# Optimization experiments

Measured on AMD Instinct MI355X. Metric: run time of the kernel, lower is better.

## Reference

```python
import jax, jax.numpy as jnp
import numpy as np

N = 20000          # num_nodes
E = 160000         # directed edges (doubled to undirected inside reference)
NF, EF, H, OUT, K = 16, 16, 128, 16, 3


def mlp2(x, w1, b1, w2, b2):
    return jnp.maximum(x @ w1 + b1, 0.0) @ w2 + b2


def edge_agg(x, src, dst, eattr, w1, b1, w2, b2):
    # message = MLP(cat[x_i (target), x_j (source), edge_attr]); aggr='add' at target
    m = mlp2(jnp.concatenate([x[dst], x[src], eattr], axis=-1), w1, b1, w2, b2)
    return jax.ops.segment_sum(m, dst, num_segments=x.shape[0])


def tag_conv(x, src, dst, lins, bias):
    # PyG TAGConv: gcn_norm (no self loops), out = sum_k lin_k(L^k x) + bias
    n = x.shape[0]
    deg = jax.ops.segment_sum(jnp.ones_like(src, dtype=x.dtype), dst, num_segments=n)
    dis = jnp.where(deg > 0, jax.lax.rsqrt(deg), 0.0)
    norm = dis[src] * dis[dst]                     # [E]
    out = x @ lins[0]
    h = x
    for k in range(1, lins.shape[0]):
        h = jax.ops.segment_sum(norm[:, None] * h[src], dst, num_segments=n)
        out = out + h @ lins[k]
    return out + bias


def setup_inputs() -> dict:
    key = jax.random.key(0)
    ks = jax.random.split(key, 20)
    s = 0.05
    lin = lambda k, i, o: jax.random.normal(k, (i, o), jnp.float32) * s
    inp = {}
    inp["x"] = jax.random.normal(ks[0], (N, NF), jnp.float32)
    inp["mask"] = (jax.random.uniform(ks[1], (N, NF)) > 0.5).astype(jnp.float32)
    inp["edge_attr"] = jax.random.normal(ks[2], (E, EF), jnp.float32)
    inp["edge_index"] = jax.random.randint(ks[3], (2, E), 0, N)
    inp["m_w1"] = lin(ks[4], NF, H); inp["m_b1"] = jnp.zeros(H)
    inp["m_w2"] = lin(ks[5], H, NF); inp["m_b2"] = jnp.zeros(NF)
    inp["ea0_w1"] = lin(ks[6], 2 * NF + EF, H); inp["ea0_b1"] = jnp.zeros(H)
    inp["ea0_w2"] = lin(ks[7], H, H); inp["ea0_b2"] = jnp.zeros(H)
    inp["tag0_w"] = jax.random.normal(ks[8], (K + 1, H, H), jnp.float32) * s
    inp["tag0_b"] = jnp.zeros(H)
    inp["ea1_w1"] = lin(ks[9], 2 * H + EF, H); inp["ea1_b1"] = jnp.zeros(H)
    inp["ea1_w2"] = lin(ks[10], H, H); inp["ea1_b2"] = jnp.zeros(H)
    inp["tag1_w"] = jax.random.normal(ks[11], (K + 1, H, H), jnp.float32) * s
    inp["tag1_b"] = jnp.zeros(H)
    inp["ea2_w1"] = lin(ks[12], 2 * H + EF, H); inp["ea2_b1"] = jnp.zeros(H)
    inp["ea2_w2"] = lin(ks[13], H, OUT); inp["ea2_b2"] = jnp.zeros(OUT)
    return inp


def reference(x, mask, edge_attr, m_w1, m_b1, m_w2, m_b2,
              ea0_w1, ea0_b1, ea0_w2, ea0_b2, tag0_w, tag0_b,
              ea1_w1, ea1_b1, ea1_w2, ea1_b2, tag1_w, tag1_b,
              ea2_w1, ea2_b1, ea2_w2, ea2_b2, edge_index):
    # undirect_graph: random directed edges -> duplicate reversed copies
    src0, dst0 = edge_index[0], edge_index[1]
    src = jnp.concatenate([src0, dst0])
    dst = jnp.concatenate([dst0, src0])
    ea = jnp.concatenate([edge_attr, edge_attr], axis=0)
    # mask embedding + residual
    h = mlp2(mask, m_w1, m_b1, m_w2, m_b2) + x
    # [EA, TAG, EA, TAG] with ReLU (dropout = identity in eval)
    h = jnp.maximum(edge_agg(h, src, dst, ea, ea0_w1, ea0_b1, ea0_w2, ea0_b2), 0.0)
    h = jnp.maximum(tag_conv(h, src, dst, tag0_w, tag0_b), 0.0)
    h = jnp.maximum(edge_agg(h, src, dst, ea, ea1_w1, ea1_b1, ea1_w2, ea1_b2), 0.0)
    h = jnp.maximum(tag_conv(h, src, dst, tag1_w, tag1_b), 0.0)
    # final EA (no activation)
    return edge_agg(h, src, dst, ea, ea2_w1, ea2_b1, ea2_w2, ea2_b2)
```

## Files before the change

### kernel.cpp

```cpp
#include <hip/hip_runtime.h>

typedef unsigned short u16;
typedef unsigned char u8;
typedef unsigned int u32;

using bfrag  = __attribute__((ext_vector_type(8))) short;
using f32x2  = __attribute__((ext_vector_type(2))) float;
using f32x4  = __attribute__((ext_vector_type(4))) float;
using f32x16 = __attribute__((ext_vector_type(16))) float;

__device__ __forceinline__ float b2f(u16 u) {
  union { u32 i; float f; } c; c.i = ((u32)u) << 16; return c.f;
}
__device__ __forceinline__ float bflo(u32 u) { union { u32 i; float f; } c; c.i = u << 16; return c.f; }
__device__ __forceinline__ float bfhi(u32 u) { union { u32 i; float f; } c; c.i = u & 0xffff0000u; return c.f; }
__device__ __forceinline__ u16 f2b(float f) {
  union { float f; u32 i; } c; c.f = f;
  u32 x = c.i;
  u32 r = x + 0x7fffu + ((x >> 16) & 1u);
  return (u16)(r >> 16);
}
__device__ __forceinline__ u32 packb2(float x, float y) {
  return ((u32)f2b(x)) | (((u32)f2b(y)) << 16);
}
__device__ __forceinline__ int rfl(int v) { return __builtin_amdgcn_readfirstlane(v); }

__global__ __launch_bounds__(256) void prologue(
    const float* __restrict__ ea, const int* __restrict__ eidx,
    const float* __restrict__ ea0_w1, const float* __restrict__ ea0_w2,
    const float* __restrict__ tag0_w, const float* __restrict__ ea1_w1,
    const float* __restrict__ ea1_w2, const float* __restrict__ tag1_w,
    const float* __restrict__ ea2_w1,
    u8* __restrict__ P0, u8* __restrict__ P1, u8* __restrict__ P2,
    int* __restrict__ degi, u16* __restrict__ Wt, int E, int N,
    int PB, int CB, int EB) {
  int t = threadIdx.x;
  if (blockIdx.x < (unsigned)PB) {
    __shared__ u16 Alds[256 * 16];
    __shared__ u16 Wlds[2048];
    int tab = blockIdx.x / EB;
    int chunk = blockIdx.x - tab * EB;
    int base = chunk * 256;
    int rows = E - base; if (rows > 256) rows = 256;
    const float* wsrc = (tab == 0) ? (ea0_w1 + 32 * 128)
                      : (tab == 1) ? (ea1_w1 + 256 * 128)
                                   : (ea2_w1 + 256 * 128);
    u8* P = (tab == 0) ? P0 : (tab == 1) ? P1 : P2;
#pragma unroll
    for (int i = 0; i < 8; ++i) {
      int idx = i * 256 + t;
      int n = idx >> 4, k = idx & 15;
      Wlds[idx] = f2b(wsrc[k * 128 + n]);
    }
#pragma unroll
    for (int i = 0; i < 4; ++i) {
      int idx = (i * 256 + t) * 4;
      float4 v = make_float4(0.f, 0.f, 0.f, 0.f);
      if ((idx >> 4) < rows) v = *(const float4*)(ea + (size_t)base * 16 + idx);
      ushort4 h;
      h.x = f2b(v.x); h.y = f2b(v.y); h.z = f2b(v.z); h.w = f2b(v.w);
      *(ushort4*)(Alds + idx) = h;
    }
    __syncthreads();
    int wave = t >> 6, lane = t & 63;
    int mm = lane & 31, kh = lane >> 5;
    bfrag b00 = *(const bfrag*)(Wlds + (2 * mm) * 16 + kh * 8);
    bfrag b01 = *(const bfrag*)(Wlds + (2 * mm + 1) * 16 + kh * 8);
    bfrag b10 = *(const bfrag*)(Wlds + (64 + 2 * mm) * 16 + kh * 8);
    bfrag b11 = *(const bfrag*)(Wlds + (64 + 2 * mm + 1) * 16 + kh * 8);
#pragma unroll
    for (int it = 0; it < 4; ++it) {
      int task = wave + it * 4;
      int rowt = (task >> 1) * 32;
      int ch = task & 1;
      int colt = ch * 64;
      bfrag a = *(const bfrag*)(Alds + (rowt + mm) * 16 + kh * 8);
      f32x16 acc0, acc1;
#pragma unroll
      for (int z = 0; z < 16; ++z) { acc0[z] = 0.f; acc1[z] = 0.f; }
      acc0 = __builtin_amdgcn_mfma_f32_32x32x16_bf16(a, ch ? b10 : b00, acc0, 0, 0, 0);
      acc1 = __builtin_amdgcn_mfma_f32_32x32x16_bf16(a, ch ? b11 : b01, acc1, 0, 0, 0);
#pragma unroll
      for (int reg = 0; reg < 16; ++reg) {
        int row = rowt + (reg & 3) + 8 * (reg >> 2) + 4 * kh;
        if (row < rows) {
          u32 pk = (u32)__builtin_amdgcn_cvt_pk_fp8_f32(acc0[reg], acc1[reg], 0, false);
          *(u16*)(P + (size_t)(base + row) * 128 + colt + 2 * mm) = (u16)pk;
        }
      }
    }
    return;
  }
  if (blockIdx.x < (unsigned)(PB + CB)) {
    int e = (blockIdx.x - PB) * 256 + t;
    if (e < E) {
      atomicAdd(&degi[eidx[E + e]], 1);
      atomicAdd(&degi[eidx[e]], 1);
    }
    return;
  }
  int wb = blockIdx.x - PB - CB;
  int mat = wb >> 3, chunk = wb & 7;
  const float* src;
  if      (mat == 0)  src = ea0_w2;
  else if (mat <= 4)  src = tag0_w + (mat - 1) * 16384;
  else if (mat == 5)  src = ea1_w1;
  else if (mat == 6)  src = ea1_w1 + 16384;
  else if (mat == 7)  src = ea1_w2;
  else if (mat <= 11) src = tag1_w + (mat - 8) * 16384;
  else if (mat == 12) src = ea2_w1;
  else                src = ea2_w1 + 16384;
  u16* dst = Wt + mat * 16384;
  for (int i = 0; i < 8; ++i) {
    int idx = chunk * 2048 + i * 256 + t;
    int k = idx >> 7, n = idx & 127;
    dst[n * 128 + k] = f2b(src[idx]);
  }
}

__global__ __launch_bounds__(256) void scan1(const int* __restrict__ degi,
                                             int* __restrict__ bsum, int N) {
  __shared__ int sh[256];
  int t = threadIdx.x;
  int gid = blockIdx.x * 256 + t;
  sh[t] = (gid < N) ? degi[gid] : 0;
  __syncthreads();
  for (int off = 128; off > 0; off >>= 1) {
    if (t < off) sh[t] += sh[t + off];
    __syncthreads();
  }
  if (t == 0) bsum[blockIdx.x] = sh[0];
}

__global__ __launch_bounds__(256) void scan23(const int* __restrict__ degi,
                                              const int* __restrict__ bsum,
                                              int* __restrict__ rowptr,
                                              int* __restrict__ cursor,
                                              float* __restrict__ dis, int nb, int N) {
  __shared__ int sh[256];
  int t = threadIdx.x;
  int v = (t < nb) ? bsum[t] : 0;
  sh[t] = v;
  __syncthreads();
  for (int off = 1; off < 256; off <<= 1) {
    int x = sh[t];
    int add = (t >= off) ? sh[t - off] : 0;
    __syncthreads();
    sh[t] = x + add;
    __syncthreads();
  }
  int blockoff = (blockIdx.x == 0) ? 0 : sh[blockIdx.x - 1];
  int total = sh[nb - 1];
  __syncthreads();
  int gid = blockIdx.x * 256 + t;
  int d = (gid < N) ? degi[gid] : 0;
  sh[t] = d;
  __syncthreads();
  for (int off = 1; off < 256; off <<= 1) {
    int x = sh[t];
    int add = (t >= off) ? sh[t - off] : 0;
    __syncthreads();
    sh[t] = x + add;
    __syncthreads();
  }
  if (gid < N) {
    int run = blockoff + sh[t] - d;
    rowptr[gid] = run;
    cursor[gid] = run;
    dis[gid] = d > 0 ? rsqrtf((float)d) : 0.0f;
  }
  if (blockIdx.x == 0 && t == 0) rowptr[N] = total;
}

__global__ __launch_bounds__(256) void fill_head(
    const int* __restrict__ eidx, int* __restrict__ cursor,
    const float* __restrict__ dis, int4* __restrict__ cr, int E,
    const float* __restrict__ mask, const float* __restrict__ x,
    const float* __restrict__ m_w1, const float* __restrict__ m_b1,
    const float* __restrict__ m_w2, const float* __restrict__ m_b2,
    const float* __restrict__ ea0_w1, const float* __restrict__ ea0_b1,
    u16* __restrict__ pb, u16* __restrict__ q, int M, int FB) {
  int t = threadIdx.x;
  if (blockIdx.x < (unsigned)FB) {
    int i = blockIdx.x * 256 + t;
    int E2 = 2 * E;
    if (i >= E2) return;
    int e = (i < E) ? i : i - E;
    int s, d;
    if (i < E) { s = eidx[e]; d = eidx[E + e]; }
    else       { s = eidx[E + e]; d = eidx[e]; }
    int pos = atomicAdd(&cursor[d], 1);
    cr[pos] = make_int4(s, e, __float_as_int(dis[s]), 0);
    return;
  }
  __shared__ float Ml[16 * 16];
  __shared__ float T1[16 * 128];
  __shared__ float H[16 * 16];
  int base = (blockIdx.x - FB) * 16;
  {
    int r = t >> 4, k = t & 15;
    int row = base + r;
    Ml[t] = (row < M) ? mask[(size_t)row * 16 + k] : 0.f;
  }
  __syncthreads();
  {
    int col = t & 127, h2 = t >> 7;
    float acc[8];
    float b1v = m_b1[col];
#pragma unroll
    for (int r = 0; r < 8; ++r) acc[r] = b1v;
    for (int k = 0; k < 16; ++k) {
      float w = m_w1[k * 128 + col];
#pragma unroll
      for (int r = 0; r < 8; ++r) acc[r] += Ml[(h2 * 8 + r) * 16 + k] * w;
    }
#pragma unroll
    for (int r = 0; r < 8; ++r) T1[(h2 * 8 + r) * 128 + col] = fmaxf(acc[r], 0.f);
  }
  __syncthreads();
  {
    int r = t >> 4, u = t & 15;
    float acc = m_b2[u];
    for (int k = 0; k < 128; ++k) acc += T1[r * 128 + k] * m_w2[k * 16 + u];
    int row = base + r;
    float xv = (row < M) ? x[(size_t)row * 16 + u] : 0.f;
    H[t] = acc + xv;
  }
  __syncthreads();
  {
    int col = t & 127, h2 = t >> 7;
    float aP[8], aQ[8];
    float b1v = ea0_b1[col];
#pragma unroll
    for (int r = 0; r < 8; ++r) { aP[r] = b1v; aQ[r] = 0.f; }
    for (int k = 0; k < 16; ++k) {
      float wd = ea0_w1[k * 128 + col];
      float ws = ea0_w1[(16 + k) * 128 + col];
#pragma unroll
      for (int r = 0; r < 8; ++r) {
        float h = H[(h2 * 8 + r) * 16 + k];
        aP[r] += h * wd;
        aQ[r] += h * ws;
      }
    }
#pragma unroll
    for (int r = 0; r < 8; ++r) {
      int row = base + h2 * 8 + r;
      if (row < M) {
        pb[(size_t)row * 128 + col] = f2b(aP[r]);
        q[(size_t)row * 128 + col]  = f2b(aQ[r]);
      }
    }
  }
}

__global__ __launch_bounds__(256) void gemm_mfma_dual(
    const u16* __restrict__ A, const u16* __restrict__ W0t, const u16* __restrict__ W1t,
    u16* __restrict__ C0, u16* __restrict__ C1, const float* __restrict__ bias0, int M) {
  __shared__ u16 Alds[64 * 136];
  __shared__ u16 Wlds[128 * 136];
  int t = threadIdx.x;
  int base = blockIdx.x * 64;
#pragma unroll
  for (int i = 0; i < 8; ++i) {
    int idx = (i * 256 + t) * 8;
    int n = idx >> 7, k = idx & 127;
    uint4 v = *(const uint4*)(W0t + idx);
    *(uint4*)(Wlds + n * 136 + k) = v;
  }
#pragma unroll
  for (int i = 0; i < 4; ++i) {
    int idx = (i * 256 + t) * 8;
    int r = idx >> 7, k = idx & 127;
    int row = base + r;
    uint4 v = make_uint4(0, 0, 0, 0);
    if (row < M) v = *(const uint4*)(A + (size_t)row * 128 + k);
    *(uint4*)(Alds + r * 136 + k) = v;
  }
  __syncthreads();
  int wave = t >> 6, lane = t & 63;
  int m = lane & 15, quad = lane >> 4;
  int arow = wave * 16 + m;
  bfrag a[4];
#pragma unroll
  for (int ks = 0; ks < 4; ++ks)
    a[ks] = *(const bfrag*)(Alds + arow * 136 + ks * 32 + quad * 8);
  f32x4 acc0[8], acc1[8];
#pragma unroll
  for (int nt = 0; nt < 8; ++nt) { acc0[nt] = (f32x4){0,0,0,0}; acc1[nt] = (f32x4){0,0,0,0}; }
#pragma unroll
  for (int nt = 0; nt < 8; ++nt) {
    int n = nt * 16 + m;
#pragma unroll
    for (int ks = 0; ks < 4; ++ks) {
      bfrag b = *(const bfrag*)(Wlds + n * 136 + ks * 32 + quad * 8);
      acc0[nt] = __builtin_amdgcn_mfma_f32_16x16x32_bf16(a[ks], b, acc0[nt], 0, 0, 0);
    }
  }
  __syncthreads();
#pragma unroll
  for (int i = 0; i < 8; ++i) {
    int idx = (i * 256 + t) * 8;
    int n = idx >> 7, k = idx & 127;
    uint4 v = *(const uint4*)(W1t + idx);
    *(uint4*)(Wlds + n * 136 + k) = v;
  }
  __syncthreads();
#pragma unroll
  for (int nt = 0; nt < 8; ++nt) {
    int n = nt * 16 + m;
#pragma unroll
    for (int ks = 0; ks < 4; ++ks) {
      bfrag b = *(const bfrag*)(Wlds + n * 136 + ks * 32 + quad * 8);
      acc1[nt] = __builtin_amdgcn_mfma_f32_16x16x32_bf16(a[ks], b, acc1[nt], 0, 0, 0);
    }
  }
#pragma unroll
  for (int nt = 0; nt < 8; ++nt) {
    int col = nt * 16 + m;
#pragma unroll
    for (int r = 0; r < 4; ++r) {
      int row = base + wave * 16 + quad * 4 + r;
      if (row < M) {
        float v0 = acc0[nt][r];
        if (bias0) v0 += bias0[col];
        C0[(size_t)row * 128 + col] = f2b(v0);
        C1[(size_t)row * 128 + col] = f2b(acc1[nt][r]);
      }
    }
  }
}

__global__ __launch_bounds__(256) void gemm_mfma_penta(
    const u16* __restrict__ A, const u16* __restrict__ W2t, const u16* __restrict__ Wt4,
    const float* __restrict__ bias, const int* __restrict__ degi,
    u16* __restrict__ G0, u16* __restrict__ G1,
    u16* __restrict__ G2, u16* __restrict__ G3, int M) {
  __shared__ u16 Alds[64 * 136];
  __shared__ u16 Wlds[128 * 136];
  int t = threadIdx.x;
  int base = blockIdx.x * 64;
#pragma unroll
  for (int i = 0; i < 8; ++i) {
    int idx = (i * 256 + t) * 8;
    int n = idx >> 7, k = idx & 127;
    uint4 v = *(const uint4*)(W2t + idx);
    *(uint4*)(Wlds + n * 136 + k) = v;
  }
#pragma unroll
  for (int i = 0; i < 4; ++i) {
    int idx = (i * 256 + t) * 8;
    int r = idx >> 7, k = idx & 127;
    int row = base + r;
    uint4 v = make_uint4(0, 0, 0, 0);
    if (row < M) v = *(const uint4*)(A + (size_t)row * 128 + k);
    *(uint4*)(Alds + r * 136 + k) = v;
  }
  __syncthreads();
  int wave = t >> 6, lane = t & 63;
  int m = lane & 15, quad = lane >> 4;
  int arow = wave * 16 + m;
  bfrag a[4];
#pragma unroll
  for (int ks = 0; ks < 4; ++ks)
    a[ks] = *(const bfrag*)(Alds + arow * 136 + ks * 32 + quad * 8);
  {
    f32x4 acc[8];
#pragma unroll
    for (int nt = 0; nt < 8; ++nt) acc[nt] = (f32x4){0.f, 0.f, 0.f, 0.f};
#pragma unroll
    for (int nt = 0; nt < 8; ++nt) {
      int n = nt * 16 + m;
#pragma unroll
      for (int ks = 0; ks < 4; ++ks) {
        bfrag b = *(const bfrag*)(Wlds + n * 136 + ks * 32 + quad * 8);
        acc[nt] = __builtin_amdgcn_mfma_f32_16x16x32_bf16(a[ks], b, acc[nt], 0, 0, 0);
      }
    }
#pragma unroll
    for (int nt = 0; nt < 8; ++nt) {
      int col = nt * 16 + m;
#pragma unroll
      for (int r = 0; r < 4; ++r) {
        int lrow = wave * 16 + quad * 4 + r;
        int row = base + lrow;
        float v = 0.f;
        if (row < M) v = fmaxf(acc[nt][r] + bias[col] * (float)degi[row], 0.f);
        Alds[lrow * 136 + col] = f2b(v);
      }
    }
  }
#pragma unroll
  for (int ks = 0; ks < 4; ++ks)
    a[ks] = *(const bfrag*)(Alds + arow * 136 + ks * 32 + quad * 8);
#pragma unroll
  for (int mat = 0; mat < 4; ++mat) {
    __syncthreads();
#pragma unroll
    for (int i = 0; i < 8; ++i) {
      int idx = (i * 256 + t) * 8;
      int n = idx >> 7, k = idx & 127;
      uint4 v = *(const uint4*)(Wt4 + mat * 16384 + idx);
      *(uint4*)(Wlds + n * 136 + k) = v;
    }
    __syncthreads();
    f32x4 acc[8];
#pragma unroll
    for (int nt = 0; nt < 8; ++nt) acc[nt] = (f32x4){0.f, 0.f, 0.f, 0.f};
#pragma unroll
    for (int nt = 0; nt < 8; ++nt) {
      int n = nt * 16 + m;
#pragma unroll
      for (int ks = 0; ks < 4; ++ks) {
        bfrag b = *(const bfrag*)(Wlds + n * 136 + ks * 32 + quad * 8);
        acc[nt] = __builtin_amdgcn_mfma_f32_16x16x32_bf16(a[ks], b, acc[nt], 0, 0, 0);
      }
    }
    u16* G = (mat == 0) ? G0 : (mat == 1) ? G1 : (mat == 2) ? G2 : G3;
#pragma unroll
    for (int nt = 0; nt < 8; ++nt) {
      int col = nt * 16 + m;
#pragma unroll
      for (int r = 0; r < 4; ++r) {
        int row = base + wave * 16 + quad * 4 + r;
        if (row < M) G[(size_t)row * 128 + col] = f2b(acc[nt][r]);
      }
    }
  }
}

__global__ __launch_bounds__(128) void gemm_tail(
    const u16* __restrict__ A, const float* __restrict__ W, float* __restrict__ Cout,
    const float* __restrict__ bias, const int* __restrict__ degi, int M) {
  const int ROWS = 8;
  int t = threadIdx.x;
  int base = blockIdx.x * ROWS;
  __shared__ float Al[ROWS * 128];
  for (int i = t; i < ROWS * 128; i += 128) {
    int r = i >> 7, k = i & 127;
    int row = base + r;
    Al[i] = (row < M) ? b2f(A[(size_t)row * 128 + k]) : 0.f;
  }
  __syncthreads();
  int r = t >> 4, u = t & 15;
  int row = base + r;
  float acc = 0.f;
  for (int k = 0; k < 128; ++k) acc += Al[r * 128 + k] * W[k * 16 + u];
  if (row < M) {
    Cout[(size_t)row * 16 + u] = acc + bias[u] * (float)degi[row];
  }
}

__device__ __forceinline__ void tag_edge(const int4* __restrict__ rr, int j,
    const u16* __restrict__ g, int lane, float& x0, float& x1) {
  int4 r = rr[j];
  int s = rfl(r.x); float w = __uint_as_float(rfl(r.z));
  u32 h = *((const u32*)(g + (size_t)s * 128) + lane);
  x0 += w * bflo(h); x1 += w * bfhi(h);
}
__device__ __forceinline__ void ea_edge(const int4* __restrict__ rr, int j,
    const u16* __restrict__ q, const u8* __restrict__ P8, int lane,
    float pb0, float pb1, float& x0, float& x1) {
  int4 r = rr[j];
  int s = rfl(r.x), i = rfl(r.y);
  u32 qv = *((const u32*)(q + (size_t)s * 128) + lane);
  u16 pv = *((const u16*)(P8 + (size_t)i * 128) + lane);
  f32x2 pf = __builtin_amdgcn_cvt_pk_f32_fp8((int)pv, false);
  x0 += fmaxf(pb0 + bflo(qv) + pf.x, 0.f);
  x1 += fmaxf(pb1 + bfhi(qv) + pf.y, 0.f);
}

template<bool FINAL>
__global__ __launch_bounds__(256) void tag_gather9(
    const u16* __restrict__ g, const u16* __restrict__ Cin,
    const float* __restrict__ bias, const float* __restrict__ dis,
    const int* __restrict__ rowptr, const int4* __restrict__ cr,
    u16* __restrict__ out, int N) {
  __shared__ int4 recs[4][64];
  int wave = threadIdx.x >> 6, lane = threadIdx.x & 63;
  int node = blockIdx.x * 4 + wave;
  if (node >= N) return;
  int e0 = rfl(rowptr[node]);
  int e1 = rfl(rowptr[node + 1]);
  int4* rr = recs[wave];
  float a0 = 0, a1 = 0, b0 = 0, b1 = 0;
  for (int base = e0; base < e1; base += 64) {
    if (base + lane < e1) rr[lane] = cr[base + lane];
    int cnt = min(64, e1 - base);
    int j = 0;
    for (; j + 8 <= cnt; j += 8) {
      tag_edge(rr, j + 0, g, lane, a0, a1);
      tag_edge(rr, j + 1, g, lane, b0, b1);
      tag_edge(rr, j + 2, g, lane, a0, a1);
      tag_edge(rr, j + 3, g, lane, b0, b1);
      tag_edge(rr, j + 4, g, lane, a0, a1);
      tag_edge(rr, j + 5, g, lane, b0, b1);
      tag_edge(rr, j + 6, g, lane, a0, a1);
      tag_edge(rr, j + 7, g, lane, b0, b1);
    }
    for (; j + 2 <= cnt; j += 2) {
      tag_edge(rr, j + 0, g, lane, a0, a1);
      tag_edge(rr, j + 1, g, lane, b0, b1);
    }
    if (j < cnt) tag_edge(rr, j, g, lane, a0, a1);
  }
  float dn = dis[node];
  float r0v = dn * (a0 + b0), r1v = dn * (a1 + b1);
  u32 cin = *((const u32*)(Cin + (size_t)node * 128) + lane);
  r0v += bflo(cin); r1v += bfhi(cin);
  if (FINAL) {
    float2 bv = *(const float2*)(bias + 2 * lane);
    r0v = fmaxf(r0v + bv.x, 0.f);
    r1v = fmaxf(r1v + bv.y, 0.f);
  }
  *((u32*)(out + (size_t)node * 128) + lane) = packb2(r0v, r1v);
}

__global__ __launch_bounds__(256) void ea_gather10(
    const u16* __restrict__ pb, const u16* __restrict__ q,
    const u8* __restrict__ P ,
    const int* __restrict__ rowptr, const int4* __restrict__ cr,
    u16* __restrict__ Hsum, int N) {
  __shared__ int4 recs[4][64];
  int wave = threadIdx.x >> 6, lane = threadIdx.x & 63;
  int node = blockIdx.x * 4 + wave;
  if (node >= N) return;
  int e0 = rfl(rowptr[node]);
  int e1 = rfl(rowptr[node + 1]);
  int4* rr = recs[wave];
  u32 pbu = *((const u32*)(pb + (size_t)node * 128) + lane);
  float pb0 = bflo(pbu), pb1 = bfhi(pbu);
  float a0 = 0, a1 = 0, b0 = 0, b1 = 0;
  for (int base = e0; base < e1; base += 64) {
    if (base + lane < e1) rr[lane] = cr[base + lane];
    int cnt = min(64, e1 - base);
    int j = 0;
    for (; j + 8 <= cnt; j += 8) {
      ea_edge(rr, j + 0, q, P, lane, pb0, pb1, a0, a1);
      ea_edge(rr, j + 1, q, P, lane, pb0, pb1, b0, b1);
      ea_edge(rr, j + 2, q, P, lane, pb0, pb1, a0, a1);
      ea_edge(rr, j + 3, q, P, lane, pb0, pb1, b0, b1);
      ea_edge(rr, j + 4, q, P, lane, pb0, pb1, a0, a1);
      ea_edge(rr, j + 5, q, P, lane, pb0, pb1, b0, b1);
      ea_edge(rr, j + 6, q, P, lane, pb0, pb1, a0, a1);
      ea_edge(rr, j + 7, q, P, lane, pb0, pb1, b0, b1);
    }
    for (; j + 2 <= cnt; j += 2) {
      ea_edge(rr, j + 0, q, P, lane, pb0, pb1, a0, a1);
      ea_edge(rr, j + 1, q, P, lane, pb0, pb1, b0, b1);
    }
    if (j < cnt) ea_edge(rr, j, q, P, lane, pb0, pb1, a0, a1);
  }
  *((u32*)(Hsum + (size_t)node * 128) + lane) = packb2(a0 + b0, a1 + b1);
}

extern "C" void kernel_launch(void* const* d_in, const int* in_sizes, int n_in,
                              void* d_out, int out_size, void* d_ws, size_t ws_size,
                              hipStream_t stream) {
  const float* x      = (const float*)d_in[0];
  const float* mask   = (const float*)d_in[1];
  const float* ea     = (const float*)d_in[2];
  const int*   eidx   = (const int*)d_in[3];
  const float* m_w1   = (const float*)d_in[4];
  const float* m_b1   = (const float*)d_in[5];
  const float* m_w2   = (const float*)d_in[6];
  const float* m_b2   = (const float*)d_in[7];
  const float* ea0_w1 = (const float*)d_in[8];
  const float* ea0_b1 = (const float*)d_in[9];
  const float* ea0_w2 = (const float*)d_in[10];
  const float* ea0_b2 = (const float*)d_in[11];
  const float* tag0_w = (const float*)d_in[12];
  const float* tag0_b = (const float*)d_in[13];
  const float* ea1_w1 = (const float*)d_in[14];
  const float* ea1_b1 = (const float*)d_in[15];
  const float* ea1_w2 = (const float*)d_in[16];
  const float* ea1_b2 = (const float*)d_in[17];
  const float* tag1_w = (const float*)d_in[18];
  const float* tag1_b = (const float*)d_in[19];
  const float* ea2_w1 = (const float*)d_in[20];
  const float* ea2_b1 = (const float*)d_in[21];
  const float* ea2_w2 = (const float*)d_in[22];
  const float* ea2_b2 = (const float*)d_in[23];

  const int N = in_sizes[0] / 16;
  const int E = in_sizes[2] / 16;
  const int E2 = 2 * E;
  const int NB = (N + 255) / 256;

  char* w = (char*)d_ws;
  auto alloc = [&](size_t bytes) { char* p = w; w += (bytes + 255) & ~(size_t)255; return p; };
  int*   degi   = (int*)alloc((size_t)N * 4);
  int*   cursor = (int*)alloc((size_t)N * 4);
  int*   rowptr = (int*)alloc((size_t)(N + 1) * 4);
  int*   bsum   = (int*)alloc((size_t)256 * 4);
  float* dis    = (float*)alloc((size_t)N * 4);
  int4*  cr     = (int4*)alloc((size_t)E2 * 16);
  u16*   X0     = (u16*)alloc((size_t)N * 128 * 2);
  u16*   X1     = (u16*)alloc((size_t)N * 128 * 2);
  u16*   X2     = (u16*)alloc((size_t)N * 128 * 2);
  u16*   G0     = (u16*)alloc((size_t)N * 128 * 2);
  u16*   G1     = (u16*)alloc((size_t)N * 128 * 2);
  u16*   G2     = (u16*)alloc((size_t)N * 128 * 2);
  u16*   G3     = (u16*)alloc((size_t)N * 128 * 2);
  u16*   Wt     = (u16*)alloc((size_t)14 * 16384 * 2);
  u8*    P0     = (u8*)alloc((size_t)E * 128);
  u8*    P1     = (u8*)alloc((size_t)E * 128);
  u8*    P2     = (u8*)alloc((size_t)E * 128);
  (void)ws_size; (void)n_in; (void)out_size;

  const int EB = (E + 255) / 256;
  const int PB = 3 * EB;
  const int CB = (E + 255) / 256;
  const int FB = (E2 + 255) / 256;
  const int HB = (N + 15) / 16;
  const int gm = (N + 63) / 64;
  const int g4 = (N + 3) / 4;
  const int gb = (N + 7) / 8;

  u16* WT_ea0w2  = Wt + 0 * 16384;
  u16* WT_tag0   = Wt + 1 * 16384;
  u16* WT_ea1d   = Wt + 5 * 16384;
  u16* WT_ea1s   = Wt + 6 * 16384;
  u16* WT_ea1w2  = Wt + 7 * 16384;
  u16* WT_tag1   = Wt + 8 * 16384;
  u16* WT_ea2d   = Wt + 12 * 16384;
  u16* WT_ea2s   = Wt + 13 * 16384;

  hipMemsetAsync(degi, 0, (size_t)N * 4, stream);
  prologue<<<PB + CB + 112, 256, 0, stream>>>(ea, eidx, ea0_w1, ea0_w2, tag0_w,
                                              ea1_w1, ea1_w2, tag1_w, ea2_w1,
                                              P0, P1, P2, degi, Wt, E, N, PB, CB, EB);
  scan1<<<NB, 256, 0, stream>>>(degi, bsum, N);
  scan23<<<NB, 256, 0, stream>>>(degi, bsum, rowptr, cursor, dis, NB, N);
  fill_head<<<FB + HB, 256, 0, stream>>>(eidx, cursor, dis, cr, E,
                                         mask, x, m_w1, m_b1, m_w2, m_b2,
                                         ea0_w1, ea0_b1, X0, X1, N, FB);

  ea_gather10<<<g4, 256, 0, stream>>>(X0, X1, P0, rowptr, cr, X2, N);
  gemm_mfma_penta<<<gm, 256, 0, stream>>>(X2, WT_ea0w2, WT_tag0, ea0_b2, degi,
                                          G0, G1, G2, G3, N);
  tag_gather9<false><<<g4, 256, 0, stream>>>(G3, G2, nullptr, dis, rowptr, cr, X1, N);
  tag_gather9<false><<<g4, 256, 0, stream>>>(X1, G1, nullptr, dis, rowptr, cr, X2, N);
  tag_gather9<true><<<g4, 256, 0, stream>>>(X2, G0, tag0_b, dis, rowptr, cr, X0, N);

  gemm_mfma_dual<<<gm, 256, 0, stream>>>(X0, WT_ea1d, WT_ea1s, X1, X2, ea1_b1, N);
  ea_gather10<<<g4, 256, 0, stream>>>(X1, X2, P1, rowptr, cr, G0, N);
  gemm_mfma_penta<<<gm, 256, 0, stream>>>(G0, WT_ea1w2, WT_tag1, ea1_b2, degi,
                                          G0, G1, G2, G3, N);
  tag_gather9<false><<<g4, 256, 0, stream>>>(G3, G2, nullptr, dis, rowptr, cr, X1, N);
  tag_gather9<false><<<g4, 256, 0, stream>>>(X1, G1, nullptr, dis, rowptr, cr, X2, N);
  tag_gather9<true><<<g4, 256, 0, stream>>>(X2, G0, tag1_b, dis, rowptr, cr, X0, N);

  gemm_mfma_dual<<<gm, 256, 0, stream>>>(X0, WT_ea2d, WT_ea2s, X1, X2, ea2_b1, N);
  ea_gather10<<<g4, 256, 0, stream>>>(X1, X2, P2, rowptr, cr, G0, N);
  gemm_tail<<<gb, 128, 0, stream>>>(G0, ea2_w2, (float*)d_out, ea2_b2, degi, N);
}
```

Before: 389.1 us.

## Move degree counting ahead and merge edge-MLP precompute into CSR fill kernel

Degree counting is split into its own small kernel that runs first. The heavy edge-attribute projection tables (P0/P1/P2) and the weight transposes move out of the prologue and into a single merged kernel together with CSR fill and the head MLP, which runs after the scans. The aim is to shorten the serial critical path: the scans now wait only on the cheap atomic degree pass instead of the large edge-GEMM prologue. Folding the GEMM work into the fill launch removes one launch and overlaps independent work. The cost is a heterogeneous mega-kernel whose shared-memory footprint applies to every block.

```diff
diff --git a/kernel.cpp b/kernel.cpp
--- a/kernel.cpp
+++ b/kernel.cpp
@@ -25,15 +25,83 @@
 }
 __device__ __forceinline__ int rfl(int v) { return __builtin_amdgcn_readfirstlane(v); }
 
-__global__ __launch_bounds__(256) void prologue(
+__global__ __launch_bounds__(256) void count_deg(const int* __restrict__ eidx,
+                                                 int* __restrict__ degi, int E) {
+  int e = blockIdx.x * 256 + threadIdx.x;
+  if (e >= E) return;
+  atomicAdd(&degi[eidx[E + e]], 1);
+  atomicAdd(&degi[eidx[e]], 1);
+}
+
+__global__ __launch_bounds__(256) void scan1(const int* __restrict__ degi,
+                                             int* __restrict__ bsum, int N) {
+  __shared__ int sh[256];
+  int t = threadIdx.x;
+  int gid = blockIdx.x * 256 + t;
+  sh[t] = (gid < N) ? degi[gid] : 0;
+  __syncthreads();
+  for (int off = 128; off > 0; off >>= 1) {
+    if (t < off) sh[t] += sh[t + off];
+    __syncthreads();
+  }
+  if (t == 0) bsum[blockIdx.x] = sh[0];
+}
+
+__global__ __launch_bounds__(256) void scan23(const int* __restrict__ degi,
+                                              const int* __restrict__ bsum,
+                                              int* __restrict__ rowptr,
+                                              int* __restrict__ cursor,
+                                              float* __restrict__ dis, int nb, int N) {
+  __shared__ int sh[256];
+  int t = threadIdx.x;
+  int v = (t < nb) ? bsum[t] : 0;
+  sh[t] = v;
+  __syncthreads();
+  for (int off = 1; off < 256; off <<= 1) {
+    int x = sh[t];
+    int add = (t >= off) ? sh[t - off] : 0;
+    __syncthreads();
+    sh[t] = x + add;
+    __syncthreads();
+  }
+  int blockoff = (blockIdx.x == 0) ? 0 : sh[blockIdx.x - 1];
+  int total = sh[nb - 1];
+  __syncthreads();
+  int gid = blockIdx.x * 256 + t;
+  int d = (gid < N) ? degi[gid] : 0;
+  sh[t] = d;
+  __syncthreads();
+  for (int off = 1; off < 256; off <<= 1) {
+    int x = sh[t];
+    int add = (t >= off) ? sh[t - off] : 0;
+    __syncthreads();
+    sh[t] = x + add;
+    __syncthreads();
+  }
+  if (gid < N) {
+    int run = blockoff + sh[t] - d;
+    rowptr[gid] = run;
+    cursor[gid] = run;
+    dis[gid] = d > 0 ? rsqrtf((float)d) : 0.0f;
+  }
+  if (blockIdx.x == 0 && t == 0) rowptr[N] = total;
+}
+
+__global__ __launch_bounds__(256) void mega(
     const float* __restrict__ ea, const int* __restrict__ eidx,
-    const float* __restrict__ ea0_w1, const float* __restrict__ ea0_w2,
+    const float* __restrict__ ea0_w1, const float* __restrict__ ea0_b1,
+    const float* __restrict__ ea0_w2,
     const float* __restrict__ tag0_w, const float* __restrict__ ea1_w1,
     const float* __restrict__ ea1_w2, const float* __restrict__ tag1_w,
     const float* __restrict__ ea2_w1,
+    const float* __restrict__ mask, const float* __restrict__ x,
+    const float* __restrict__ m_w1, const float* __restrict__ m_b1,
+    const float* __restrict__ m_w2, const float* __restrict__ m_b2,
     u8* __restrict__ P0, u8* __restrict__ P1, u8* __restrict__ P2,
-    int* __restrict__ degi, u16* __restrict__ Wt, int E, int N,
-    int PB, int CB, int EB) {
+    u16* __restrict__ Wt, int* __restrict__ cursor,
+    const float* __restrict__ dis, int4* __restrict__ cr,
+    u16* __restrict__ pb, u16* __restrict__ q,
+    int E, int N, int PB, int FB, int EB) {
   int t = threadIdx.x;
   if (blockIdx.x < (unsigned)PB) {
     __shared__ u16 Alds[256 * 16];
@@ -91,98 +159,28 @@
     }
     return;
   }
-  if (blockIdx.x < (unsigned)(PB + CB)) {
-    int e = (blockIdx.x - PB) * 256 + t;
-    if (e < E) {
-      atomicAdd(&degi[eidx[E + e]], 1);
-      atomicAdd(&degi[eidx[e]], 1);
+  if (blockIdx.x < (unsigned)(PB + 112)) {
+    int wb = blockIdx.x - PB;
+    int mat = wb >> 3, chunk = wb & 7;
+    const float* src;
+    if      (mat == 0)  src = ea0_w2;
+    else if (mat <= 4)  src = tag0_w + (mat - 1) * 16384;
+    else if (mat == 5)  src = ea1_w1;
+    else if (mat == 6)  src = ea1_w1 + 16384;
+    else if (mat == 7)  src = ea1_w2;
+    else if (mat <= 11) src = tag1_w + (mat - 8) * 16384;
+    else if (mat == 12) src = ea2_w1;
+    else                src = ea2_w1 + 16384;
+    u16* dst = Wt + mat * 16384;
+    for (int i = 0; i < 8; ++i) {
+      int idx = chunk * 2048 + i * 256 + t;
+      int k = idx >> 7, n = idx & 127;
+      dst[n * 128 + k] = f2b(src[idx]);
     }
     return;
   }
-  int wb = blockIdx.x - PB - CB;
-  int mat = wb >> 3, chunk = wb & 7;
-  const float* src;
-  if      (mat == 0)  src = ea0_w2;
-  else if (mat <= 4)  src = tag0_w + (mat - 1) * 16384;
-  else if (mat == 5)  src = ea1_w1;
-  else if (mat == 6)  src = ea1_w1 + 16384;
-  else if (mat == 7)  src = ea1_w2;
-  else if (mat <= 11) src = tag1_w + (mat - 8) * 16384;
-  else if (mat == 12) src = ea2_w1;
-  else                src = ea2_w1 + 16384;
-  u16* dst = Wt + mat * 16384;
-  for (int i = 0; i < 8; ++i) {
-    int idx = chunk * 2048 + i * 256 + t;
-    int k = idx >> 7, n = idx & 127;
-    dst[n * 128 + k] = f2b(src[idx]);
-  }
-}
-
-__global__ __launch_bounds__(256) void scan1(const int* __restrict__ degi,
-                                             int* __restrict__ bsum, int N) {
-  __shared__ int sh[256];
-  int t = threadIdx.x;
-  int gid = blockIdx.x * 256 + t;
-  sh[t] = (gid < N) ? degi[gid] : 0;
-  __syncthreads();
-  for (int off = 128; off > 0; off >>= 1) {
-    if (t < off) sh[t] += sh[t + off];
-    __syncthreads();
-  }
-  if (t == 0) bsum[blockIdx.x] = sh[0];
-}
-
-__global__ __launch_bounds__(256) void scan23(const int* __restrict__ degi,
-                                              const int* __restrict__ bsum,
-                                              int* __restrict__ rowptr,
-                                              int* __restrict__ cursor,
-                                              float* __restrict__ dis, int nb, int N) {
-  __shared__ int sh[256];
-  int t = threadIdx.x;
-  int v = (t < nb) ? bsum[t] : 0;
-  sh[t] = v;
-  __syncthreads();
-  for (int off = 1; off < 256; off <<= 1) {
-    int x = sh[t];
-    int add = (t >= off) ? sh[t - off] : 0;
-    __syncthreads();
-    sh[t] = x + add;
-    __syncthreads();
-  }
-  int blockoff = (blockIdx.x == 0) ? 0 : sh[blockIdx.x - 1];
-  int total = sh[nb - 1];
-  __syncthreads();
-  int gid = blockIdx.x * 256 + t;
-  int d = (gid < N) ? degi[gid] : 0;
-  sh[t] = d;
-  __syncthreads();
-  for (int off = 1; off < 256; off <<= 1) {
-    int x = sh[t];
-    int add = (t >= off) ? sh[t - off] : 0;
-    __syncthreads();
-    sh[t] = x + add;
-    __syncthreads();
-  }
-  if (gid < N) {
-    int run = blockoff + sh[t] - d;
-    rowptr[gid] = run;
-    cursor[gid] = run;
-    dis[gid] = d > 0 ? rsqrtf((float)d) : 0.0f;
-  }
-  if (blockIdx.x == 0 && t == 0) rowptr[N] = total;
-}
-
-__global__ __launch_bounds__(256) void fill_head(
-    const int* __restrict__ eidx, int* __restrict__ cursor,
-    const float* __restrict__ dis, int4* __restrict__ cr, int E,
-    const float* __restrict__ mask, const float* __restrict__ x,
-    const float* __restrict__ m_w1, const float* __restrict__ m_b1,
-    const float* __restrict__ m_w2, const float* __restrict__ m_b2,
-    const float* __restrict__ ea0_w1, const float* __restrict__ ea0_b1,
-    u16* __restrict__ pb, u16* __restrict__ q, int M, int FB) {
-  int t = threadIdx.x;
-  if (blockIdx.x < (unsigned)FB) {
-    int i = blockIdx.x * 256 + t;
+  if (blockIdx.x < (unsigned)(PB + 112 + FB)) {
+    int i = (blockIdx.x - PB - 112) * 256 + t;
     int E2 = 2 * E;
     if (i >= E2) return;
     int e = (i < E) ? i : i - E;
@@ -196,11 +194,11 @@
   __shared__ float Ml[16 * 16];
   __shared__ float T1[16 * 128];
   __shared__ float H[16 * 16];
-  int base = (blockIdx.x - FB) * 16;
+  int base = (blockIdx.x - PB - 112 - FB) * 16;
   {
     int r = t >> 4, k = t & 15;
     int row = base + r;
-    Ml[t] = (row < M) ? mask[(size_t)row * 16 + k] : 0.f;
+    Ml[t] = (row < N) ? mask[(size_t)row * 16 + k] : 0.f;
   }
   __syncthreads();
   {
@@ -223,7 +221,7 @@
     float acc = m_b2[u];
     for (int k = 0; k < 128; ++k) acc += T1[r * 128 + k] * m_w2[k * 16 + u];
     int row = base + r;
-    float xv = (row < M) ? x[(size_t)row * 16 + u] : 0.f;
+    float xv = (row < N) ? x[(size_t)row * 16 + u] : 0.f;
     H[t] = acc + xv;
   }
   __syncthreads();
@@ -246,7 +244,7 @@
 #pragma unroll
     for (int r = 0; r < 8; ++r) {
       int row = base + h2 * 8 + r;
-      if (row < M) {
+      if (row < N) {
         pb[(size_t)row * 128 + col] = f2b(aP[r]);
         q[(size_t)row * 128 + col]  = f2b(aQ[r]);
       }
@@ -627,14 +625,13 @@
   u16* WT_ea2s   = Wt + 13 * 16384;
 
   hipMemsetAsync(degi, 0, (size_t)N * 4, stream);
-  prologue<<<PB + CB + 112, 256, 0, stream>>>(ea, eidx, ea0_w1, ea0_w2, tag0_w,
-                                              ea1_w1, ea1_w2, tag1_w, ea2_w1,
-                                              P0, P1, P2, degi, Wt, E, N, PB, CB, EB);
+  count_deg<<<CB, 256, 0, stream>>>(eidx, degi, E);
   scan1<<<NB, 256, 0, stream>>>(degi, bsum, N);
   scan23<<<NB, 256, 0, stream>>>(degi, bsum, rowptr, cursor, dis, NB, N);
-  fill_head<<<FB + HB, 256, 0, stream>>>(eidx, cursor, dis, cr, E,
-                                         mask, x, m_w1, m_b1, m_w2, m_b2,
-                                         ea0_w1, ea0_b1, X0, X1, N, FB);
+  mega<<<PB + 112 + FB + HB, 256, 0, stream>>>(
+      ea, eidx, ea0_w1, ea0_b1, ea0_w2, tag0_w, ea1_w1, ea1_w2, tag1_w, ea2_w1,
+      mask, x, m_w1, m_b1, m_w2, m_b2,
+      P0, P1, P2, Wt, cursor, dis, cr, X0, X1, E, N, PB, FB, EB);
 
   ea_gather10<<<g4, 256, 0, stream>>>(X0, X1, P0, rowptr, cr, X2, N);
   gemm_mfma_penta<<<gm, 256, 0, stream>>>(X2, WT_ea0w2, WT_tag0, ea0_b2, degi,
```

Result: slower. 404.8 us (+4.0%).
